# Optimization experiments

Hardware: AMD Instinct MI355X
Metric: run time of the kernel (lower is better)

The kernel has to match this reference:

```python
import jax, jax.numpy as jnp
import numpy as np

B, S, F_IN, D, H, DFF, L = 64, 256, 64, 512, 8, 2048, 6
A_DIM, FEAT, OUT = 8, 32, 5
EPS = 1e-3  # keras default epsilon for BatchNorm/LayerNorm


def _sinusoidal_pes(seq_len, d_model):
    pos = np.arange(seq_len)[:, None].astype(np.float32)
    i = np.arange(d_model)[None, :].astype(np.float32)
    angle = pos / np.power(10000.0, (2.0 * np.floor(i / 2.0)) / d_model)
    pe = np.zeros((seq_len, d_model), dtype=np.float32)
    pe[:, 0::2] = np.sin(angle[:, 0::2])
    pe[:, 1::2] = np.cos(angle[:, 1::2])
    return jnp.asarray(pe)


def setup_inputs() -> dict:
    key = jax.random.key(0)
    ks = jax.random.split(key, 16)
    w = lambda k, shape: 0.02 * jax.random.normal(k, shape, dtype=jnp.float32)
    return {
        'state': jax.random.normal(ks[0], (B, S, F_IN), dtype=jnp.float32),
        'action': jax.random.normal(ks[1], (B, A_DIM), dtype=jnp.float32),
        'pes': _sinusoidal_pes(S, D),
        'W_emb': w(ks[2], (F_IN, D)), 'b_emb': jnp.zeros((D,), jnp.float32),
        'Wq': w(ks[3], (L, D, D)), 'bq': jnp.zeros((L, D), jnp.float32),
        'Wk': w(ks[4], (L, D, D)), 'bk': jnp.zeros((L, D), jnp.float32),
        'Wv': w(ks[5], (L, D, D)), 'bv': jnp.zeros((L, D), jnp.float32),
        'Wo': w(ks[6], (L, D, D)), 'bo': jnp.zeros((L, D), jnp.float32),
        'bn_gamma': jnp.ones((L, D), jnp.float32), 'bn_beta': jnp.zeros((L, D), jnp.float32),
        'W1': w(ks[7], (L, D, DFF)), 'b1': jnp.zeros((L, DFF), jnp.float32),
        'W2': w(ks[8], (L, DFF, D)), 'b2': jnp.zeros((L, D), jnp.float32),
        'ln_gamma': jnp.ones((L, D), jnp.float32), 'ln_beta': jnp.zeros((L, D), jnp.float32),
        'Wf': w(ks[9], (S * D, FEAT)), 'bf': jnp.zeros((FEAT,), jnp.float32),
        'Wfin': w(ks[10], (FEAT + A_DIM, OUT)), 'bfin': jnp.zeros((OUT,), jnp.float32),
    }


def _encoder(x, pes, layer_params):
    # x: [B, S, D]
    x = x + pes  # positional encoding

    def step(h, p):
        Wq, bq, Wk, bk, Wv, bv, Wo, bo, gb, bb, W1, b1, W2, b2, gl, bl = p
        b, s, d = h.shape
        dh = d // H
        q = (h @ Wq + bq).reshape(b, s, H, dh)
        k = (h @ Wk + bk).reshape(b, s, H, dh)
        v = (h @ Wv + bv).reshape(b, s, H, dh)
        scores = jnp.einsum('bqhd,bkhd->bhqk', q, k) / jnp.sqrt(jnp.asarray(dh, h.dtype))
        attn = jax.nn.softmax(scores, axis=-1)
        ctx = jnp.einsum('bhqk,bkhd->bqhd', attn, v).reshape(b, s, d)
        ctx = ctx @ Wo + bo
        y = h + ctx
        # BatchNormalization over (batch, seq), per-channel (training-mode batch stats)
        mu = y.mean(axis=(0, 1))
        var = y.var(axis=(0, 1))
        y = gb * (y - mu) * jax.lax.rsqrt(var + EPS) + bb
        # FFN + residual + LayerNorm
        f = jax.nn.relu(y @ W1 + b1) @ W2 + b2
        z = y + f
        mu2 = z.mean(axis=-1, keepdims=True)
        var2 = z.var(axis=-1, keepdims=True)
        z = gl * (z - mu2) * jax.lax.rsqrt(var2 + EPS) + bl
        return z, None

    x, _ = jax.lax.scan(step, x, layer_params)
    return x


def reference(state, action, pes, W_emb, b_emb, Wq, bq, Wk, bk, Wv, bv, Wo, bo,
              bn_gamma, bn_beta, W1, b1, W2, b2, ln_gamma, ln_beta, Wf, bf, Wfin, bfin):
    x = state @ W_emb + b_emb                       # [B, S, D]
    layer_params = (Wq, bq, Wk, bk, Wv, bv, Wo, bo, bn_gamma, bn_beta,
                    W1, b1, W2, b2, ln_gamma, ln_beta)
    enc = _encoder(x, pes, layer_params)            # [B, S, D]
    flat = enc.reshape(enc.shape[0], -1)            # [B, S*D]
    feat = flat @ Wf + bf                           # [B, 32]
    out = jnp.concatenate([feat, action], axis=-1) @ Wfin + bfin  # [B, 5]
    return out
```

## Files before the change

kernel.cpp:

```cpp
#include <hip/hip_runtime.h>

typedef short bf16x8 __attribute__((ext_vector_type(8)));
typedef float f32x4 __attribute__((ext_vector_type(4)));
typedef unsigned short us;

#define BN_EPS 1e-3f

static __device__ __forceinline__ us f2bs(float x) {
  unsigned int u = __builtin_bit_cast(unsigned int, x);
  unsigned int r = (u + 0x7FFFu + ((u >> 16) & 1u)) >> 16;
  return (us)r;
}
static __device__ __forceinline__ float b2f(us v) {
  unsigned int u = (unsigned int)v << 16;
  return __builtin_bit_cast(float, u);
}

static __device__ __forceinline__ void gl_lds16(const us* g, us* l) {
  __builtin_amdgcn_global_load_lds(
      (const __attribute__((address_space(1))) void*)g,
      (__attribute__((address_space(3))) void*)l, 16, 0, 0);
}

__global__ __launch_bounds__(256) void transpose_bf16(
    const float* __restrict__ src, us* __restrict__ dst, int K, int N,
    long sstride, long dstride) {
  long sbs = (long)blockIdx.z * sstride;
  long sbd = (long)blockIdx.z * dstride;
  __shared__ float tile[32][33];
  int tx = threadIdx.x & 31, ty = threadIdx.x >> 5;
  int k0 = blockIdx.x * 32, n0 = blockIdx.y * 32;
  for (int i = 0; i < 32; i += 8)
    tile[ty + i][tx] = src[sbs + (long)(k0 + ty + i) * N + n0 + tx];
  __syncthreads();
  for (int i = 0; i < 32; i += 8)
    dst[sbd + (long)(n0 + ty + i) * K + k0 + tx] = f2bs(tile[tx][ty + i]);
}

__global__ __launch_bounds__(256) void embed_kernel(
    const float* __restrict__ state, const float* __restrict__ Wemb,
    const float* __restrict__ bemb, const float* __restrict__ pes,
    us* __restrict__ hb) {
  int t = threadIdx.x;
  int row0 = blockIdx.x * 8;
  __shared__ float st[8][64];
  {
    int i = t;
    st[i >> 6][i & 63] = state[(long)row0 * 64 + i];
    i += 256;
    st[i >> 6][i & 63] = state[(long)row0 * 64 + i];
  }
  __syncthreads();
  int c0 = t, c1 = t + 256;
  float acc0[8], acc1[8];
#pragma unroll
  for (int r = 0; r < 8; ++r) { acc0[r] = 0.f; acc1[r] = 0.f; }
  for (int kk = 0; kk < 64; ++kk) {
    float w0 = Wemb[kk * 512 + c0], w1 = Wemb[kk * 512 + c1];
#pragma unroll
    for (int r = 0; r < 8; ++r) {
      acc0[r] += st[r][kk] * w0;
      acc1[r] += st[r][kk] * w1;
    }
  }
  float be0 = bemb[c0], be1 = bemb[c1];
#pragma unroll
  for (int r = 0; r < 8; ++r) {
    int row = row0 + r, s = row & 255;
    hb[(long)row * 512 + c0] = f2bs(acc0[r] + be0 + pes[(long)s * 512 + c0]);
    hb[(long)row * 512 + c1] = f2bs(acc1[r] + be1 + pes[(long)s * 512 + c1]);
  }
}

enum { EPI_QKV = 0, EPI_RESID_BF16 = 1, EPI_RELU_BF16 = 2, EPI_FFN2_BF16 = 3,
       EPI_FEAT = 4 };

template <int EPI>
__global__ __launch_bounds__(512, 2) void gemm256(
    const us* __restrict__ A, int lda, const us* __restrict__ Bt, int ldb,
    void* __restrict__ Cout, void* __restrict__ C2, void* __restrict__ C3,
    int ldc, const float* __restrict__ bias, const us* __restrict__ resid,
    const float* __restrict__ gamma, const float* __restrict__ beta, int K) {
  const int tid = threadIdx.x;
  const int w = tid >> 6, l = tid & 63;
  const int wr = w >> 2, wc = w & 3;
  const int lr = l & 15, lh = l >> 4;
  const long m0 = (long)blockIdx.x * 256;
  const long n0 = (long)blockIdx.y * 256;
  const int KC = K >> 5;
  __shared__ __align__(16) us sh[4 * 16384];
  const int o = tid * 16;
  const int lg = o ^ ((o >> 2) & 0x30);
  const int sr = lg >> 6;
  const int sc = (lg & 63) >> 1;
  const int pb = lr * 32 + ((lh * 8) ^ ((lr & 3) << 3));
  const us* Asl = sh + wr * 4096 + pb;
  const us* Bsl = sh + 8192 + (wc >> 1) * 4096 + (wc & 1) * 2048 + pb;

  for (int j = 0; j < 3; ++j) {
    us* slot = sh + j * 16384;
    gl_lds16(A + (m0 + sr) * lda + j * 32 + sc, slot + tid * 8);
    gl_lds16(A + (m0 + 128 + sr) * lda + j * 32 + sc, slot + 4096 + tid * 8);
    gl_lds16(Bt + (n0 + sr) * ldb + j * 32 + sc, slot + 8192 + tid * 8);
    gl_lds16(Bt + (n0 + 128 + sr) * ldb + j * 32 + sc, slot + 12288 + tid * 8);
  }
  asm volatile("s_waitcnt vmcnt(8)" ::: "memory");
  __builtin_amdgcn_s_barrier();

  f32x4 acc[8][4] = {};
  for (int c = 0; c < KC; ++c) {
    const int soff = (c & 3) * 16384;
    const bool st = (c + 3) < KC;
    us* nslot = sh + ((c + 3) & 3) * 16384;
    const int nk = (c + 3) * 32;
    if (st) {
      gl_lds16(A + (m0 + sr) * lda + nk + sc, nslot + tid * 8);
      gl_lds16(A + (m0 + 128 + sr) * lda + nk + sc, nslot + 4096 + tid * 8);
    }
    bf16x8 bfr[4], af[4];
#pragma unroll
    for (int ni = 0; ni < 4; ++ni)
      bfr[ni] = *(const bf16x8*)(Bsl + soff + ni * 512);
#pragma unroll
    for (int mi = 0; mi < 4; ++mi)
      af[mi] = *(const bf16x8*)(Asl + soff + mi * 512);
    __builtin_amdgcn_s_barrier();
    __builtin_amdgcn_s_setprio(1);
#pragma unroll
    for (int mi = 0; mi < 4; ++mi)
#pragma unroll
      for (int ni = 0; ni < 4; ++ni)
        acc[mi][ni] = __builtin_amdgcn_mfma_f32_16x16x32_bf16(
            af[mi], bfr[ni], acc[mi][ni], 0, 0, 0);
    __builtin_amdgcn_s_setprio(0);
    __builtin_amdgcn_s_barrier();
    if (st) {
      gl_lds16(Bt + (n0 + sr) * ldb + nk + sc, nslot + 8192 + tid * 8);
      gl_lds16(Bt + (n0 + 128 + sr) * ldb + nk + sc, nslot + 12288 + tid * 8);
    }
#pragma unroll
    for (int mi = 0; mi < 4; ++mi)
      af[mi] = *(const bf16x8*)(Asl + soff + (mi + 4) * 512);
    __builtin_amdgcn_s_barrier();
    __builtin_amdgcn_s_setprio(1);
#pragma unroll
    for (int mi = 0; mi < 4; ++mi)
#pragma unroll
      for (int ni = 0; ni < 4; ++ni)
        acc[mi + 4][ni] = __builtin_amdgcn_mfma_f32_16x16x32_bf16(
            af[mi], bfr[ni], acc[mi + 4][ni], 0, 0, 0);
    __builtin_amdgcn_s_setprio(0);
    if (c < KC - 3)
      asm volatile("s_waitcnt vmcnt(8)" ::: "memory");
    else if (c == KC - 3)
      asm volatile("s_waitcnt vmcnt(4)" ::: "memory");
    else if (c == KC - 2)
      asm volatile("s_waitcnt vmcnt(0)" ::: "memory");
    __builtin_amdgcn_s_barrier();
  }
#pragma unroll
  for (int mi = 0; mi < 8; ++mi)
#pragma unroll
    for (int ni = 0; ni < 4; ++ni) {
      const int cl = wc * 64 + ni * 16 + lr;
      const float bv_ = bias[(int)n0 + cl];
#pragma unroll
      for (int q_ = 0; q_ < 4; ++q_) {
        const int rl = wr * 128 + mi * 16 + lh * 4 + q_;
        sh[rl * 256 + cl] = f2bs(fmaxf(acc[mi][ni][q_] + bv_, 0.f));
      }
    }
  asm volatile("s_waitcnt lgkmcnt(0)" ::: "memory");
  __builtin_amdgcn_s_barrier();
  for (int i = tid; i < 8192; i += 512) {
    const int idx = i * 8;
    const int row = idx >> 8, col = idx & 255;
    *(uint4*)&((us*)Cout)[(m0 + row) * ldc + n0 + col] = *(uint4*)&sh[idx];
  }
  (void)resid; (void)C2; (void)C3; (void)gamma; (void)beta;
}

template <int BM, int BN, int WM, int WN, int EPI>
__global__ __launch_bounds__((BM / WM) * (BN / WN) * 64)
void gemm_bt(const us* __restrict__ A, int lda, long batchA,
             const us* __restrict__ Bt, int ldb, long batchB,
             void* __restrict__ Cout, void* __restrict__ C2,
             void* __restrict__ C3, int ldc,
             const float* __restrict__ bias,
             const us* __restrict__ resid,
             float* __restrict__ gsum, float* __restrict__ gsumsq,
             const float* __restrict__ gamma, const float* __restrict__ beta,
             int K) {
  constexpr int WCols = BN / WN;
  constexpr int NT = (BM / WM) * (BN / WN) * 64;
  constexpr int NW = NT / 64;
  constexpr int MI = WM / 16, NI = WN / 16;
  constexpr int LA = BM / 8;
  constexpr int LB = BN / 8;
  const int tid = threadIdx.x;
  const int w = tid >> 6, l = tid & 63;
  const int wr = w / WCols, wc = w % WCols;
  const int lr = l & 15, lh = l >> 4;
  const int z = blockIdx.z;
  const long m0 = (long)blockIdx.x * BM;
  const long n0 = (long)blockIdx.y * BN;
  A += (long)z * batchA;
  Bt += (long)z * batchB;
  __shared__ __align__(16) us smem[BM * 64 + BN * 64];
  us* Asm = smem;
  us* Bsm = smem + BM * 64;
  const int srow = l >> 3, scol = (l & 7) << 3;
  f32x4 acc[MI][NI] = {};
  for (int kt = 0; kt < K; kt += 64) {
    __syncthreads();
    for (int j = w; j < LA; j += NW) {
      int rb = j * 8;
      gl_lds16(A + (m0 + rb + srow) * lda + kt + scol, Asm + rb * 64);
    }
    for (int j = w; j < LB; j += NW) {
      int rb = j * 8;
      gl_lds16(Bt + (n0 + rb + srow) * ldb + kt + scol, Bsm + rb * 64);
    }
    asm volatile("s_waitcnt vmcnt(0)" ::: "memory");
    __syncthreads();
#pragma unroll
    for (int kk = 0; kk < 64; kk += 32) {
      bf16x8 af[MI], bfr[NI];
#pragma unroll
      for (int mi = 0; mi < MI; ++mi)
        af[mi] = *(const bf16x8*)&Asm[(wr * WM + mi * 16 + lr) * 64 + kk + lh * 8];
#pragma unroll
      for (int ni = 0; ni < NI; ++ni)
        bfr[ni] = *(const bf16x8*)&Bsm[(wc * WN + ni * 16 + lr) * 64 + kk + lh * 8];
#pragma unroll
      for (int mi = 0; mi < MI; ++mi)
#pragma unroll
        for (int ni = 0; ni < NI; ++ni)
          acc[mi][ni] = __builtin_amdgcn_mfma_f32_16x16x32_bf16(
              af[mi], bfr[ni], acc[mi][ni], 0, 0, 0);
    }
  }

  if constexpr (EPI == EPI_QKV) {
    const int seg = (int)(n0 >> 9);
    const int nc0 = (int)(n0 & 511);
    if (seg == 2) {
#pragma unroll
      for (int mi = 0; mi < MI; ++mi) {
#pragma unroll
        for (int ni = 0; ni < NI; ++ni) {
          const int segc = nc0 + wc * WN + ni * 16 + lr;
          const float bv_ = beta[segc];
          ushort4 pv;
#pragma unroll
          for (int q_ = 0; q_ < 4; ++q_)
            ((us*)&pv)[q_] = f2bs(acc[mi][ni][q_] + bv_);
          const long row0g = m0 + wr * WM + mi * 16 + lh * 4;
          const long oo = (((row0g >> 8) * 8 + (segc >> 6)) * 64 + (segc & 63)) *
                              256 + (row0g & 255);
          *(ushort4*)&((us*)C3)[oo] = pv;
        }
      }
    } else {
      __syncthreads();
#pragma unroll
      for (int mi = 0; mi < MI; ++mi)
#pragma unroll
        for (int ni = 0; ni < NI; ++ni) {
          const int cl = wc * WN + ni * 16 + lr;
          const float bv_ = seg == 0 ? bias[nc0 + cl] : gamma[nc0 + cl];
#pragma unroll
          for (int q_ = 0; q_ < 4; ++q_) {
            const int rl = wr * WM + mi * 16 + lh * 4 + q_;
            smem[rl * BN + cl] = f2bs(acc[mi][ni][q_] + bv_);
          }
        }
      __syncthreads();
      us* dstp = seg == 0 ? (us*)Cout : (us*)C2;
      for (int i = tid; i < (BM * BN) / 8; i += NT) {
        const int idx = i * 8;
        const int row = idx / BN, colc = idx % BN;
        *(uint4*)&dstp[(m0 + row) * 512 + nc0 + colc] = *(uint4*)&smem[idx];
      }
    }
  } else if constexpr ((EPI == EPI_RESID_BF16 || EPI == EPI_FFN2_BF16) &&
                       BM == 128 && BN == 128) {
    __syncthreads();
    float cs[NI] = {}, cq[NI] = {};
#pragma unroll
    for (int mi = 0; mi < MI; ++mi)
#pragma unroll
      for (int ni = 0; ni < NI; ++ni) {
        const int cl = wc * WN + ni * 16 + lr;
        const int col = (int)n0 + cl;
        const float bv_ = bias[col];
        float aa = 0.f, bb2 = 0.f;
        if constexpr (EPI == EPI_FFN2_BF16) {
          aa = gsum[col];
          bb2 = gsumsq[col];
        }
#pragma unroll
        for (int q_ = 0; q_ < 4; ++q_) {
          const int rl = wr * WM + mi * 16 + lh * 4 + q_;
          float v = acc[mi][ni][q_] + bv_;
          if constexpr (EPI == EPI_RESID_BF16) {
            v += b2f(resid[(m0 + rl) * ldc + col]);
            cs[ni] += v;
            cq[ni] += v * v;
            smem[rl * BN + cl] = f2bs(v);
          } else {
            float ybn = b2f(resid[(m0 + rl) * ldc + col]) * aa + bb2;
            smem[rl * BN + cl] = f2bs(ybn + v);
          }
        }
      }
    if constexpr (EPI == EPI_RESID_BF16) {
#pragma unroll
      for (int ni = 0; ni < NI; ++ni) {
        float s = cs[ni], qv = cq[ni];
        s += __shfl_xor(s, 16);
        qv += __shfl_xor(qv, 16);
        s += __shfl_xor(s, 32);
        qv += __shfl_xor(qv, 32);
        if (lh == 0) {
          const int col = (int)n0 + wc * WN + ni * 16 + lr;
          atomicAdd(&gsum[col], s);
          atomicAdd(&gsumsq[col], qv);
        }
      }
    }
    __syncthreads();
    for (int i = tid; i < (BM * BN) / 8; i += NT) {
      const int idx = i * 8;
      const int row = idx / BN, colc = idx % BN;
      *(uint4*)&((us*)Cout)[(m0 + row) * ldc + n0 + colc] = *(uint4*)&smem[idx];
    }
  } else {
#pragma unroll
    for (int mi = 0; mi < MI; ++mi) {
#pragma unroll
      for (int ni = 0; ni < NI; ++ni) {
        const int col = (int)n0 + wc * WN + ni * 16 + lr;
#pragma unroll
        for (int q_ = 0; q_ < 4; ++q_) {
          const long row = m0 + wr * WM + mi * 16 + lh * 4 + q_;
          if constexpr (EPI == EPI_FEAT) {
            atomicAdd(&((float*)Cout)[row * ldc + col], acc[mi][ni][q_]);
          }
        }
      }
    }
  }
}

__global__ __launch_bounds__(256) void attn_kernel(
    const us* __restrict__ q, const us* __restrict__ k,
    const us* __restrict__ vt, us* __restrict__ ctx) {
  const int half = blockIdx.x;
  const int z = blockIdx.y;
  const int b = z >> 3, hh = z & 7;
  const long qkBase = (long)b * 131072 + hh * 64;
  const int tid = threadIdx.x, w = tid >> 6, l = tid & 63;
  const int lr = l & 15, lh = l >> 4;
  __shared__ __align__(16) us Qs[32][72];
  __shared__ __align__(16) us Ks[64][72];
  __shared__ __align__(16) us Pb[32][264];
  __shared__ float fred[32][2];
  const int qr = (w >> 1) * 16, qc = (w & 1) * 32;
  const us* vb = vt + (long)z * 16384;
  const int ldr = tid >> 3, ldc = (tid & 7) << 3;

  for (int qi = 0; qi < 4; ++qi) {
    const int qb = half * 4 + qi;
    *(uint4*)&Qs[ldr][ldc] =
        *(const uint4*)(q + qkBase + (long)(qb * 32 + ldr) * 512 + ldc);
    f32x4 sacc[4][2] = {};
    for (int skb = 0; skb < 4; ++skb) {
      __syncthreads();
      for (int i = tid; i < 512; i += 256) {
        int r = i >> 3, c = (i & 7) << 3;
        *(uint4*)&Ks[r][c] =
            *(const uint4*)(k + qkBase + (long)(skb * 64 + r) * 512 + c);
      }
      __syncthreads();
#pragma unroll
      for (int kh = 0; kh < 2; ++kh) {
        bf16x8 aq = *(const bf16x8*)&Qs[qr + lr][kh * 32 + lh * 8];
#pragma unroll
        for (int ni = 0; ni < 2; ++ni) {
          bf16x8 bkk = *(const bf16x8*)&Ks[qc + ni * 16 + lr][kh * 32 + lh * 8];
          sacc[skb][ni] = __builtin_amdgcn_mfma_f32_16x16x32_bf16(
              aq, bkk, sacc[skb][ni], 0, 0, 0);
        }
      }
    }
    float m0[4] = {-1e30f, -1e30f, -1e30f, -1e30f};
#pragma unroll
    for (int skb = 0; skb < 4; ++skb)
#pragma unroll
      for (int ni = 0; ni < 2; ++ni)
#pragma unroll
        for (int q_ = 0; q_ < 4; ++q_) {
          float v = sacc[skb][ni][q_] * 0.125f;
          sacc[skb][ni][q_] = v;
          m0[q_] = fmaxf(m0[q_], v);
        }
#pragma unroll
    for (int off = 1; off < 16; off <<= 1)
#pragma unroll
      for (int q_ = 0; q_ < 4; ++q_)
        m0[q_] = fmaxf(m0[q_], __shfl_xor(m0[q_], off));
    if (lr == 0) {
#pragma unroll
      for (int q_ = 0; q_ < 4; ++q_) fred[qr + lh * 4 + q_][w & 1] = m0[q_];
    }
    __syncthreads();
#pragma unroll
    for (int q_ = 0; q_ < 4; ++q_) {
      int row = qr + lh * 4 + q_;
      m0[q_] = fmaxf(fred[row][0], fred[row][1]);
    }
    float s0[4] = {0.f, 0.f, 0.f, 0.f};
#pragma unroll
    for (int skb = 0; skb < 4; ++skb)
#pragma unroll
      for (int ni = 0; ni < 2; ++ni)
#pragma unroll
        for (int q_ = 0; q_ < 4; ++q_) {
          float e = __expf(sacc[skb][ni][q_] - m0[q_]);
          sacc[skb][ni][q_] = e;
          s0[q_] += e;
        }
#pragma unroll
    for (int off = 1; off < 16; off <<= 1)
#pragma unroll
      for (int q_ = 0; q_ < 4; ++q_) s0[q_] += __shfl_xor(s0[q_], off);
    __syncthreads();
    if (lr == 0) {
#pragma unroll
      for (int q_ = 0; q_ < 4; ++q_) fred[qr + lh * 4 + q_][w & 1] = s0[q_];
    }
    __syncthreads();
#pragma unroll
    for (int q_ = 0; q_ < 4; ++q_) {
      int row = qr + lh * 4 + q_;
      s0[q_] = 1.f / (fred[row][0] + fred[row][1]);
    }
#pragma unroll
    for (int skb = 0; skb < 4; ++skb)
#pragma unroll
      for (int ni = 0; ni < 2; ++ni)
#pragma unroll
        for (int q_ = 0; q_ < 4; ++q_)
          Pb[qr + lh * 4 + q_][skb * 64 + qc + ni * 16 + lr] =
              f2bs(sacc[skb][ni][q_] * s0[q_]);
    f32x4 pacc[2] = {};
    for (int kc = 0; kc < 256; kc += 64) {
      __syncthreads();
      for (int i = tid; i < 512; i += 256) {
        int r = i >> 3, c = (i & 7) << 3;
        *(uint4*)&Ks[r][c] = *(const uint4*)(vb + (long)r * 256 + kc + c);
      }
      __syncthreads();
#pragma unroll
      for (int kh = 0; kh < 2; ++kh) {
        bf16x8 ap = *(const bf16x8*)&Pb[qr + lr][kc + kh * 32 + lh * 8];
#pragma unroll
        for (int ni = 0; ni < 2; ++ni) {
          bf16x8 bv2 = *(const bf16x8*)&Ks[qc + ni * 16 + lr][kh * 32 + lh * 8];
          pacc[ni] = __builtin_amdgcn_mfma_f32_16x16x32_bf16(
              ap, bv2, pacc[ni], 0, 0, 0);
        }
      }
    }
    const long cb2 = ((long)(b * 256 + qb * 32)) * 512 + hh * 64;
#pragma unroll
    for (int ni = 0; ni < 2; ++ni)
#pragma unroll
      for (int q_ = 0; q_ < 4; ++q_) {
        int row = qr + lh * 4 + q_;
        int col = qc + ni * 16 + lr;
        ctx[cb2 + (long)row * 512 + col] = f2bs(pacc[ni][q_]);
      }
  }
}

__global__ void bn_coef(float* __restrict__ gsum, float* __restrict__ gsumsq,
                        const float* __restrict__ gamma,
                        const float* __restrict__ beta) {
  int c = blockIdx.x * 256 + threadIdx.x;
  if (c < 512) {
    const float invN = 1.f / 16384.f;
    float mu = gsum[c] * invN;
    float var = gsumsq[c] * invN - mu * mu;
    float a = gamma[c] * rsqrtf(var + BN_EPS);
    float b = beta[c] - mu * a;
    gsum[c] = a;
    gsumsq[c] = b;
  }
}

__global__ __launch_bounds__(256) void fold_w1(
    const us* __restrict__ W1T, const float* __restrict__ aa,
    const float* __restrict__ bb, const float* __restrict__ b1,
    us* __restrict__ W1s, float* __restrict__ bias1f) {
  int n = blockIdx.x * 4 + (threadIdx.x >> 6);
  int l = threadIdx.x & 63;
  int k0 = l * 8;
  const us* row = W1T + (long)n * 512;
  us tmp[8], outv[8];
  *(uint4*)tmp = *(const uint4*)(row + k0);
  float dot = 0.f;
#pragma unroll
  for (int j = 0; j < 8; ++j) {
    float wv = b2f(tmp[j]);
    dot += bb[k0 + j] * wv;
    outv[j] = f2bs(aa[k0 + j] * wv);
  }
  *(uint4*)(W1s + (long)n * 512 + k0) = *(uint4*)outv;
  for (int off = 32; off >= 1; off >>= 1) dot += __shfl_down(dot, off);
  if (l == 0) bias1f[n] = b1[n] + dot;
}

__global__ __launch_bounds__(128) void ln_kernel(
    const us* __restrict__ zin, const float* __restrict__ g,
    const float* __restrict__ b, us* __restrict__ hb,
    float* __restrict__ gsum, float* __restrict__ gsumsq) {
  int r = blockIdx.x, t = threadIdx.x;
  if (r == 0) {
    for (int i = t; i < 512; i += 128) {
      gsum[i] = 0.f;
      gsumsq[i] = 0.f;
    }
  }
  const us* zr = zin + (long)r * 512;
  ushort4 vz = *(const ushort4*)(zr + t * 4);
  float v0 = b2f(((us*)&vz)[0]), v1 = b2f(((us*)&vz)[1]);
  float v2 = b2f(((us*)&vz)[2]), v3 = b2f(((us*)&vz)[3]);
  float s = v0 + v1 + v2 + v3;
  float qs = v0 * v0 + v1 * v1 + v2 * v2 + v3 * v3;
  for (int off = 32; off >= 1; off >>= 1) {
    s += __shfl_down(s, off);
    qs += __shfl_down(qs, off);
  }
  __shared__ float ls[2], lq[2];
  if ((t & 63) == 0) {
    ls[t >> 6] = s;
    lq[t >> 6] = qs;
  }
  __syncthreads();
  float mu = (ls[0] + ls[1]) * (1.f / 512.f);
  float var = (lq[0] + lq[1]) * (1.f / 512.f) - mu * mu;
  float rs = rsqrtf(var + BN_EPS);
  float4 gg = *(const float4*)(g + t * 4);
  float4 bb = *(const float4*)(b + t * 4);
  ushort4 hv;
  ((us*)&hv)[0] = f2bs(gg.x * (v0 - mu) * rs + bb.x);
  ((us*)&hv)[1] = f2bs(gg.y * (v1 - mu) * rs + bb.y);
  ((us*)&hv)[2] = f2bs(gg.z * (v2 - mu) * rs + bb.z);
  ((us*)&hv)[3] = f2bs(gg.w * (v3 - mu) * rs + bb.w);
  *(ushort4*)(hb + (long)r * 512 + t * 4) = hv;
}

__global__ void zerof(float* __restrict__ p, int n) {
  int i = blockIdx.x * 256 + threadIdx.x;
  if (i < n) p[i] = 0.f;
}

__global__ __launch_bounds__(320) void final_head(
    const float* __restrict__ feat, const float* __restrict__ bf_,
    const float* __restrict__ action, const float* __restrict__ Wfin,
    const float* __restrict__ bfin, float* __restrict__ out) {
  int t = threadIdx.x;
  int b = t & 63, o = t >> 6;
  float acc = bfin[o];
  for (int j = 0; j < 32; ++j) acc += (feat[b * 32 + j] + bf_[j]) * Wfin[j * 5 + o];
  for (int j = 0; j < 8; ++j) acc += action[b * 8 + j] * Wfin[(32 + j) * 5 + o];
  out[b * 5 + o] = acc;
}

extern "C" void kernel_launch(void* const* d_in, const int* in_sizes, int n_in,
                              void* d_out, int out_size, void* d_ws,
                              size_t ws_size, hipStream_t stream) {
  const float* state = (const float*)d_in[0];
  const float* action = (const float*)d_in[1];
  const float* pes = (const float*)d_in[2];
  const float* W_emb = (const float*)d_in[3];
  const float* b_emb = (const float*)d_in[4];
  const float* Wq = (const float*)d_in[5];
  const float* bq = (const float*)d_in[6];
  const float* Wk = (const float*)d_in[7];
  const float* bk = (const float*)d_in[8];
  const float* Wv = (const float*)d_in[9];
  const float* bv = (const float*)d_in[10];
  const float* Wo = (const float*)d_in[11];
  const float* bo = (const float*)d_in[12];
  const float* bn_g = (const float*)d_in[13];
  const float* bn_b = (const float*)d_in[14];
  const float* W1 = (const float*)d_in[15];
  const float* b1 = (const float*)d_in[16];
  const float* W2 = (const float*)d_in[17];
  const float* b2 = (const float*)d_in[18];
  const float* ln_g = (const float*)d_in[19];
  const float* ln_b = (const float*)d_in[20];
  const float* Wf = (const float*)d_in[21];
  const float* bf_ = (const float*)d_in[22];
  const float* Wfin = (const float*)d_in[23];
  const float* bfin = (const float*)d_in[24];
  float* out = (float*)d_out;
  (void)in_sizes; (void)n_in; (void)out_size;

  char* wp = (char*)d_ws;
  size_t off = 0;
  auto take = [&](size_t bytes) {
    void* p = wp + off;
    off += (bytes + 255) & ~(size_t)255;
    return p;
  };
  us* qkvT = (us*)take(6ull * 1536 * 512 * 2);
  us* WoT = (us*)take(6ull * 512 * 512 * 2);
  us* W1T = (us*)take(6ull * 2048 * 512 * 2);
  us* W2T = (us*)take(6ull * 512 * 2048 * 2);
  us* WfT = (us*)take(32ull * 131072 * 2);
  us* hb = (us*)take(16384ull * 512 * 2);
  us* ybf = (us*)take(16384ull * 512 * 2);
  us* W1s = (us*)take(2048ull * 512 * 2);
  float* bias1f = (float*)take(2048 * 4);
  us* qb_ = (us*)take(16384ull * 512 * 2);
  us* kb_ = (us*)take(16384ull * 512 * 2);
  us* vt = (us*)take(16384ull * 512 * 2);
  us* bigR4 = (us*)take(33554432ull * 2);
  float* gsum = (float*)take(512 * 4);
  float* gsumsq = (float*)take(512 * 4);
  float* feat = (float*)take(2048 * 4);
  us* ctxb = bigR4;
  us* f1 = bigR4;
  us* zbf = qb_;

  if (off > ws_size) return;

  transpose_bf16<<<dim3(16, 16, 6), 256, 0, stream>>>(Wq, qkvT, 512, 512,
                                                      262144, 786432);
  transpose_bf16<<<dim3(16, 16, 6), 256, 0, stream>>>(Wk, qkvT + 262144, 512,
                                                      512, 262144, 786432);
  transpose_bf16<<<dim3(16, 16, 6), 256, 0, stream>>>(Wv, qkvT + 524288, 512,
                                                      512, 262144, 786432);
  transpose_bf16<<<dim3(16, 16, 6), 256, 0, stream>>>(Wo, WoT, 512, 512,
                                                      262144, 262144);
  transpose_bf16<<<dim3(16, 64, 6), 256, 0, stream>>>(W1, W1T, 512, 2048,
                                                      1048576, 1048576);
  transpose_bf16<<<dim3(64, 16, 6), 256, 0, stream>>>(W2, W2T, 2048, 512,
                                                      1048576, 1048576);
  transpose_bf16<<<dim3(4096, 1, 1), 256, 0, stream>>>(Wf, WfT, 131072, 32,
                                                       0, 0);
  embed_kernel<<<2048, 256, 0, stream>>>(state, W_emb, b_emb, pes, hb);
  zerof<<<4, 256, 0, stream>>>(gsum, 1024);

  for (int l = 0; l < 6; ++l) {
    const us* qkvTl = qkvT + (size_t)l * 786432;
    const us* WoTl = WoT + (size_t)l * 262144;
    const us* W1Tl = W1T + (size_t)l * 1048576;
    const us* W2Tl = W2T + (size_t)l * 1048576;

    gemm_bt<128, 128, 64, 64, EPI_QKV><<<dim3(128, 12, 1), 256, 0, stream>>>(
        hb, 512, 0, qkvTl, 512, 0, qb_, kb_, vt, 512, bq + l * 512,
        nullptr, nullptr, nullptr, bk + l * 512, bv + l * 512, 512);
    attn_kernel<<<dim3(2, 512), 256, 0, stream>>>(qb_, kb_, vt, ctxb);
    gemm_bt<128, 128, 64, 64, EPI_RESID_BF16><<<dim3(128, 4, 1), 256, 0, stream>>>(
        ctxb, 512, 0, WoTl, 512, 0, ybf, nullptr, nullptr, 512, bo + l * 512,
        hb, gsum, gsumsq, nullptr, nullptr, 512);
    bn_coef<<<2, 256, 0, stream>>>(gsum, gsumsq, bn_g + l * 512,
                                   bn_b + l * 512);
    fold_w1<<<512, 256, 0, stream>>>(W1Tl, gsum, gsumsq, b1 + l * 2048, W1s,
                                     bias1f);
    gemm256<EPI_RELU_BF16><<<dim3(64, 8), 512, 0, stream>>>(
        ybf, 512, W1s, 512, f1, nullptr, nullptr, 2048, bias1f, nullptr,
        nullptr, nullptr, 512);
    gemm_bt<128, 128, 64, 64, EPI_FFN2_BF16><<<dim3(128, 4, 1), 256, 0, stream>>>(
        f1, 2048, 0, W2Tl, 2048, 0, zbf, nullptr, nullptr, 512, b2 + l * 512,
        ybf, gsum, gsumsq, nullptr, nullptr, 2048);
    ln_kernel<<<16384, 128, 0, stream>>>(zbf, ln_g + l * 512, ln_b + l * 512,
                                         hb, gsum, gsumsq);
  }

  zerof<<<8, 256, 0, stream>>>(feat, 2048);
  gemm_bt<64, 32, 32, 16, EPI_FEAT><<<dim3(1, 1, 128), 256, 0, stream>>>(
      hb, 131072, 1024, WfT, 131072, 1024, feat, nullptr, nullptr, 32,
      nullptr, nullptr, nullptr, nullptr, nullptr, nullptr, 1024);
  final_head<<<1, 320, 0, stream>>>(feat, bf_, action, Wfin, bfin, out);
}
```

Before: 1.516 ms.

## Add dedicated 256x128 pipelined GEMM kernel for FFN2 with fused BN-residual epilogue

Replaces the generic 128x128 gemm_bt used for the FFN second matmul (K=2048) with a specialised 256x128-tile kernel. It uses 512 threads, a 4-slot LDS ring filled by direct global-to-LDS loads with explicit vmcnt waits, swizzled LDS addressing, split MFMA phases with setprio, and the same BN-residual epilogue. The larger tile raises arithmetic intensity and the deeper prefetch hides load latency. In exchange the grid shrinks to 256 blocks and each block holds 96KB of LDS, which may limit occupancy.

```diff
diff --git a/kernel.cpp b/kernel.cpp
--- a/kernel.cpp
+++ b/kernel.cpp
@@ -178,6 +178,110 @@
     *(uint4*)&((us*)Cout)[(m0 + row) * ldc + n0 + col] = *(uint4*)&sh[idx];
   }
   (void)resid; (void)C2; (void)C3; (void)gamma; (void)beta;
+}
+
+__global__ __launch_bounds__(512, 2) void gemm256x128_ffn2(
+    const us* __restrict__ A, int lda, const us* __restrict__ Bt, int ldb,
+    us* __restrict__ Cout, int ldc, const float* __restrict__ bias,
+    const us* __restrict__ resid, const float* __restrict__ gsA,
+    const float* __restrict__ gsB, int K) {
+  const int tid = threadIdx.x;
+  const int w = tid >> 6, l = tid & 63;
+  const int wr = w >> 1, wc = w & 1;
+  const int lr = l & 15, lh = l >> 4;
+  const long m0 = (long)blockIdx.x * 256;
+  const long n0 = (long)blockIdx.y * 128;
+  const int KC = K >> 5;
+  __shared__ __align__(16) us sh[4 * 12288];
+  const int o = tid * 16;
+  const int lg = o ^ ((o >> 2) & 0x30);
+  const int sr = lg >> 6;
+  const int sc = (lg & 63) >> 1;
+  const int pb = lr * 32 + ((lh * 8) ^ ((lr & 3) << 3));
+  const us* Asl = sh + wr * 2048 + pb;
+  const us* Bsl = sh + 8192 + wc * 2048 + pb;
+
+  for (int j = 0; j < 3; ++j) {
+    us* slot = sh + j * 12288;
+    gl_lds16(A + (m0 + sr) * lda + j * 32 + sc, slot + tid * 8);
+    gl_lds16(A + (m0 + 128 + sr) * lda + j * 32 + sc, slot + 4096 + tid * 8);
+    gl_lds16(Bt + (n0 + sr) * ldb + j * 32 + sc, slot + 8192 + tid * 8);
+  }
+  asm volatile("s_waitcnt vmcnt(6)" ::: "memory");
+  __builtin_amdgcn_s_barrier();
+
+  f32x4 acc[4][4] = {};
+  for (int c = 0; c < KC; ++c) {
+    const int soff = (c & 3) * 12288;
+    const bool st = (c + 3) < KC;
+    us* nslot = sh + ((c + 3) & 3) * 12288;
+    const int nk = (c + 3) * 32;
+    if (st) {
+      gl_lds16(A + (m0 + sr) * lda + nk + sc, nslot + tid * 8);
+      gl_lds16(A + (m0 + 128 + sr) * lda + nk + sc, nslot + 4096 + tid * 8);
+    }
+    bf16x8 bfr[4], af[2];
+#pragma unroll
+    for (int ni = 0; ni < 4; ++ni)
+      bfr[ni] = *(const bf16x8*)(Bsl + soff + ni * 512);
+#pragma unroll
+    for (int mi = 0; mi < 2; ++mi)
+      af[mi] = *(const bf16x8*)(Asl + soff + mi * 512);
+    __builtin_amdgcn_s_barrier();
+    __builtin_amdgcn_s_setprio(1);
+#pragma unroll
+    for (int mi = 0; mi < 2; ++mi)
+#pragma unroll
+      for (int ni = 0; ni < 4; ++ni)
+        acc[mi][ni] = __builtin_amdgcn_mfma_f32_16x16x32_bf16(
+            af[mi], bfr[ni], acc[mi][ni], 0, 0, 0);
+    __builtin_amdgcn_s_setprio(0);
+    __builtin_amdgcn_s_barrier();
+    if (st) {
+      gl_lds16(Bt + (n0 + sr) * ldb + nk + sc, nslot + 8192 + tid * 8);
+    }
+#pragma unroll
+    for (int mi = 0; mi < 2; ++mi)
+      af[mi] = *(const bf16x8*)(Asl + soff + (mi + 2) * 512);
+    __builtin_amdgcn_s_barrier();
+    __builtin_amdgcn_s_setprio(1);
+#pragma unroll
+    for (int mi = 0; mi < 2; ++mi)
+#pragma unroll
+      for (int ni = 0; ni < 4; ++ni)
+        acc[mi + 2][ni] = __builtin_amdgcn_mfma_f32_16x16x32_bf16(
+            af[mi], bfr[ni], acc[mi + 2][ni], 0, 0, 0);
+    __builtin_amdgcn_s_setprio(0);
+    if (c < KC - 3)
+      asm volatile("s_waitcnt vmcnt(6)" ::: "memory");
+    else if (c == KC - 3)
+      asm volatile("s_waitcnt vmcnt(3)" ::: "memory");
+    else if (c == KC - 2)
+      asm volatile("s_waitcnt vmcnt(0)" ::: "memory");
+    __builtin_amdgcn_s_barrier();
+  }
+#pragma unroll
+  for (int mi = 0; mi < 4; ++mi)
+#pragma unroll
+    for (int ni = 0; ni < 4; ++ni) {
+      const int cl = wc * 64 + ni * 16 + lr;
+      const int col = (int)n0 + cl;
+      const float bv_ = bias[col];
+      const float aa = gsA[col], bb2 = gsB[col];
+#pragma unroll
+      for (int q_ = 0; q_ < 4; ++q_) {
+        const int rl = wr * 64 + mi * 16 + lh * 4 + q_;
+        float ybn = b2f(resid[(m0 + rl) * ldc + col]) * aa + bb2;
+        sh[rl * 128 + cl] = f2bs(ybn + acc[mi][ni][q_] + bv_);
+      }
+    }
+  asm volatile("s_waitcnt lgkmcnt(0)" ::: "memory");
+  __builtin_amdgcn_s_barrier();
+  for (int i = tid; i < 4096; i += 512) {
+    const int idx = i * 8;
+    const int row = idx >> 7, col = idx & 127;
+    *(uint4*)&Cout[(m0 + row) * ldc + n0 + col] = *(uint4*)&sh[idx];
+  }
 }
 
 template <int BM, int BN, int WM, int WN, int EPI>
@@ -283,8 +387,7 @@
         *(uint4*)&dstp[(m0 + row) * 512 + nc0 + colc] = *(uint4*)&smem[idx];
       }
     }
-  } else if constexpr ((EPI == EPI_RESID_BF16 || EPI == EPI_FFN2_BF16) &&
-                       BM == 128 && BN == 128) {
+  } else if constexpr (EPI == EPI_RESID_BF16 && BM == 128 && BN == 128) {
     __syncthreads();
     float cs[NI] = {}, cq[NI] = {};
 #pragma unroll
@@ -294,39 +397,26 @@
         const int cl = wc * WN + ni * 16 + lr;
         const int col = (int)n0 + cl;
         const float bv_ = bias[col];
-        float aa = 0.f, bb2 = 0.f;
-        if constexpr (EPI == EPI_FFN2_BF16) {
-          aa = gsum[col];
-          bb2 = gsumsq[col];
-        }
 #pragma unroll
         for (int q_ = 0; q_ < 4; ++q_) {
           const int rl = wr * WM + mi * 16 + lh * 4 + q_;
-          float v = acc[mi][ni][q_] + bv_;
-          if constexpr (EPI == EPI_RESID_BF16) {
-            v += b2f(resid[(m0 + rl) * ldc + col]);
-            cs[ni] += v;
-            cq[ni] += v * v;
-            smem[rl * BN + cl] = f2bs(v);
-          } else {
-            float ybn = b2f(resid[(m0 + rl) * ldc + col]) * aa + bb2;
-            smem[rl * BN + cl] = f2bs(ybn + v);
-          }
+          float v = acc[mi][ni][q_] + bv_ + b2f(resid[(m0 + rl) * ldc + col]);
+          cs[ni] += v;
+          cq[ni] += v * v;
+          smem[rl * BN + cl] = f2bs(v);
         }
       }
-    if constexpr (EPI == EPI_RESID_BF16) {
-#pragma unroll
-      for (int ni = 0; ni < NI; ++ni) {
-        float s = cs[ni], qv = cq[ni];
-        s += __shfl_xor(s, 16);
-        qv += __shfl_xor(qv, 16);
-        s += __shfl_xor(s, 32);
-        qv += __shfl_xor(qv, 32);
-        if (lh == 0) {
-          const int col = (int)n0 + wc * WN + ni * 16 + lr;
-          atomicAdd(&gsum[col], s);
-          atomicAdd(&gsumsq[col], qv);
-        }
+#pragma unroll
+    for (int ni = 0; ni < NI; ++ni) {
+      float s = cs[ni], qv = cq[ni];
+      s += __shfl_xor(s, 16);
+      qv += __shfl_xor(qv, 16);
+      s += __shfl_xor(s, 32);
+      qv += __shfl_xor(qv, 32);
+      if (lh == 0) {
+        const int col = (int)n0 + wc * WN + ni * 16 + lr;
+        atomicAdd(&gsum[col], s);
+        atomicAdd(&gsumsq[col], qv);
       }
     }
     __syncthreads();
@@ -676,9 +766,8 @@
     gemm256<EPI_RELU_BF16><<<dim3(64, 8), 512, 0, stream>>>(
         ybf, 512, W1s, 512, f1, nullptr, nullptr, 2048, bias1f, nullptr,
         nullptr, nullptr, 512);
-    gemm_bt<128, 128, 64, 64, EPI_FFN2_BF16><<<dim3(128, 4, 1), 256, 0, stream>>>(
-        f1, 2048, 0, W2Tl, 2048, 0, zbf, nullptr, nullptr, 512, b2 + l * 512,
-        ybf, gsum, gsumsq, nullptr, nullptr, 2048);
+    gemm256x128_ffn2<<<dim3(64, 4), 512, 0, stream>>>(
+        f1, 2048, W2Tl, 2048, zbf, 512, b2 + l * 512, ybf, gsum, gsumsq, 2048);
     ln_kernel<<<16384, 128, 0, stream>>>(zbf, ln_g + l * 512, ln_b + l * 512,
                                          hb, gsum, gsumsq);
   }
```

After: 1.432 ms. 1.06x faster.
